# Kernel tuning notes

Hardware: AMD Instinct MI355X
Metric: run time of the kernel (lower is better)

## Reference

```python
import jax, jax.numpy as jnp
import numpy as np

N = 50000      # nodes
E = 800000     # edges (before self-loops)
B = 512        # graphs in batch
IN, HID, OUT, HEADS = 768, 256, 128, 4
NEG_SLOPE = 0.2
EPS = 1e-16


def glorot(key, shape):
    fan = shape[0] + shape[-1]
    return jax.random.normal(key, shape, jnp.float32) * jnp.sqrt(2.0 / fan)


def setup_inputs() -> dict:
    key = jax.random.key(0)
    ks = jax.random.split(key, 12)
    d1, d2 = HID // HEADS, OUT // HEADS
    return {
        "x": jax.random.normal(ks[0], (N, IN), jnp.float32),
        "edge_index": jax.random.randint(ks[1], (2, E), 0, N),
        "batch": jnp.sort(jax.random.randint(ks[2], (N,), 0, B)),
        # conv1: GATConv(IN, HID//HEADS, heads=HEADS)
        "W1": glorot(ks[3], (IN, HID)),
        "att_src1": glorot(ks[4], (HEADS, d1)),
        "att_dst1": glorot(ks[5], (HEADS, d1)),
        "b1": jnp.zeros((HID,), jnp.float32),
        # conv2: GATConv(HID+IN, OUT//HEADS, heads=HEADS)
        "W2": glorot(ks[6], (HID + IN, OUT)),
        "att_src2": glorot(ks[7], (HEADS, d2)),
        "att_dst2": glorot(ks[8], (HEADS, d2)),
        "b2": jnp.zeros((OUT,), jnp.float32),
    }


def gat_conv(x, src, dst, W, att_src, att_dst, bias):
    # PyG GATConv (concat heads): h = x @ W, e_ij = LeakyReLU(a_s.h_j + a_d.h_i),
    # alpha = softmax over incoming edges of each destination node.
    n = x.shape[0]
    heads, d = att_src.shape
    h = (x @ W).reshape(n, heads, d)                          # [N,H,D]
    a_s = jnp.einsum('nhd,hd->nh', h, att_src)                # [N,H]
    a_d = jnp.einsum('nhd,hd->nh', h, att_dst)
    e = jax.nn.leaky_relu(a_s[src] + a_d[dst], NEG_SLOPE)     # [Etot,H]
    e_max = jax.ops.segment_max(e, dst, num_segments=n)
    e = jnp.exp(e - e_max[dst])
    denom = jax.ops.segment_sum(e, dst, num_segments=n)
    alpha = e / (denom[dst] + EPS)                            # [Etot,H]
    msg = h[src] * alpha[:, :, None]                          # [Etot,H,D]
    out = jax.ops.segment_sum(msg, dst, num_segments=n)       # [N,H,D]
    return out.reshape(n, heads * d) + bias


def reference(x, edge_index, batch, W1, att_src1, att_dst1, b1,
              W2, att_src2, att_dst2, b2):
    # BUrumorGAT swaps edge direction: row<->col
    src = edge_index[1]
    dst = edge_index[0]
    # PyG GATConv adds self-loops by default
    loops = jnp.arange(N)
    src = jnp.concatenate([src, loops])
    dst = jnp.concatenate([dst, loops])

    x1 = x  # original features
    h1 = gat_conv(x, src, dst, W1, att_src1, att_dst1, b1)    # [N,HID]
    x2 = h1

    # root of each graph = first node (in order) with that batch id
    roots = jax.ops.segment_min(jnp.arange(N), batch, num_segments=B)  # [B]
    re1 = x1[roots[batch]]                                    # [N,IN]
    xc = jax.nn.relu(jnp.concatenate([h1, re1], axis=1))      # [N,HID+IN]
    # F.dropout with training=False is identity (eval mode)

    h2 = jax.nn.relu(gat_conv(xc, src, dst, W2, att_src2, att_dst2, b2))  # [N,OUT]
    re2 = x2[roots[batch]]                                    # [N,HID]
    feat = jnp.concatenate([h2, re2], axis=1)                 # [N,OUT+HID]

    counts = jax.ops.segment_sum(jnp.ones((N,), jnp.float32), batch, num_segments=B)
    pooled = jax.ops.segment_sum(feat, batch, num_segments=B)
    return pooled / jnp.clip(counts, 1.0)[:, None]            # [B,OUT+HID]
```

## Files before the change

kernel.cpp:

```cpp
#include <hip/hip_runtime.h>

#define NN 50000
#define NBGRAPH 512
#define DIN 768
#define DHID 256
#define DOUT 128

typedef unsigned short ushort_t;
typedef __attribute__((ext_vector_type(4))) float f32x4;
typedef _Float16 f16_t;
typedef __attribute__((ext_vector_type(8))) _Float16 f16x8;

__device__ __forceinline__ float lrelu(float v) { return v > 0.f ? v : 0.2f * v; }

__device__ __forceinline__ float h2f_u(ushort_t u) { return (float)__builtin_bit_cast(f16_t, u); }
__device__ __forceinline__ ushort_t f2h_u(float f) { return __builtin_bit_cast(ushort_t, (f16_t)f); }

__device__ __forceinline__ float sel_h(int h, float q0, float q1, float q2, float q3) {
  float lo = (h & 1) ? q1 : q0;
  float hi = (h & 1) ? q3 : q2;
  return (h & 2) ? hi : lo;
}

__device__ __forceinline__ f16x8 cvt8(float4 u, float4 v) {
  unsigned int a = __builtin_bit_cast(unsigned int, __builtin_amdgcn_cvt_pkrtz(u.x, u.y));
  unsigned int b = __builtin_bit_cast(unsigned int, __builtin_amdgcn_cvt_pkrtz(u.z, u.w));
  unsigned int c = __builtin_bit_cast(unsigned int, __builtin_amdgcn_cvt_pkrtz(v.x, v.y));
  unsigned int d = __builtin_bit_cast(unsigned int, __builtin_amdgcn_cvt_pkrtz(v.z, v.w));
  uint4 q = {a, b, c, d};
  return __builtin_bit_cast(f16x8, q);
}
__device__ __forceinline__ f16x8 cvt8_relu(float4 u, float4 v) {
  u.x = fmaxf(u.x, 0.f); u.y = fmaxf(u.y, 0.f); u.z = fmaxf(u.z, 0.f); u.w = fmaxf(u.w, 0.f);
  v.x = fmaxf(v.x, 0.f); v.y = fmaxf(v.y, 0.f); v.z = fmaxf(v.z, 0.f); v.w = fmaxf(v.w, 0.f);
  return cvt8(u, v);
}

__device__ __forceinline__ void gl_lds16(const void* g, void* l) {
  __builtin_amdgcn_global_load_lds(
      (const __attribute__((address_space(1))) unsigned int*)g,
      (__attribute__((address_space(3))) unsigned int*)l, 16, 0, 0);
}

__global__ void k_zero2(int* __restrict__ a, int* __restrict__ b, int n) {
  int i = blockIdx.x * blockDim.x + threadIdx.x;
  if (i < n) { a[i] = 0; b[i] = 0; }
}

__global__ void k_hist(const int* __restrict__ ei, int* __restrict__ deg, int E, int Etot) {
  int e = blockIdx.x * blockDim.x + threadIdx.x;
  if (e >= Etot) return;
  int dst = (e < E) ? ei[e] : (e - E);
  atomicAdd(&deg[dst], 1);
}

__global__ __launch_bounds__(1024) void k_scan1(const int* __restrict__ deg, int* __restrict__ off,
                                                int* __restrict__ bsum, int n) {
  __shared__ int wsum[16];
  int tid = threadIdx.x, lane = tid & 63, w = tid >> 6;
  int i = blockIdx.x * 1024 + tid;
  int v = (i < n) ? deg[i] : 0;
  int x = v;
#pragma unroll
  for (int d = 1; d < 64; d <<= 1) { int t = __shfl_up(x, d); if (lane >= d) x += t; }
  if (lane == 63) wsum[w] = x;
  __syncthreads();
  if (tid < 16) {
    int y = wsum[tid];
#pragma unroll
    for (int d = 1; d < 16; d <<= 1) { int t = __shfl_up(y, d); if (tid >= d) y += t; }
    wsum[tid] = y;
  }
  __syncthreads();
  int base = (w > 0) ? wsum[w - 1] : 0;
  if (i < n) off[i] = base + x - v;
  if (tid == 1023) bsum[blockIdx.x] = wsum[15];
}

__global__ void k_scan2(int* __restrict__ bsum, int* __restrict__ off, int nb, int n) {
  int lane = threadIdx.x;
  int v = (lane < nb) ? bsum[lane] : 0;
  int x = v;
#pragma unroll
  for (int d = 1; d < 64; d <<= 1) { int t = __shfl_up(x, d); if (lane >= d) x += t; }
  if (lane < nb) bsum[lane] = x - v;
  if (lane == 63) off[n] = x;
}

__global__ void k_scan3(int* __restrict__ off, const int* __restrict__ bsum, int n) {
  int i = blockIdx.x * blockDim.x + threadIdx.x;
  if (i < n) off[i] += bsum[i >> 10];
}

__global__ void k_scatter(const int* __restrict__ ei, const int* __restrict__ off,
                          int* __restrict__ cur, int* __restrict__ csr, int E, int Etot) {
  int e = blockIdx.x * blockDim.x + threadIdx.x;
  if (e >= Etot) return;
  int dst, src;
  if (e < E) { dst = ei[e]; src = ei[E + e]; }
  else       { dst = src = e - E; }
  int p = atomicAdd(&cur[dst], 1);
  csr[off[dst] + p] = src;
}

__global__ void k_segstart(const int* __restrict__ batch, int* __restrict__ segstart, int n, int b_cnt) {
  int b = blockIdx.x * blockDim.x + threadIdx.x;
  if (b > b_cnt) return;
  int lo = 0, hi = n;
  while (lo < hi) { int mid = (lo + hi) >> 1; if (batch[mid] < b) lo = mid + 1; else hi = mid; }
  segstart[b] = lo;
}

__global__ void k_rootn(const int* __restrict__ batch, const int* __restrict__ segstart,
                        int* __restrict__ rootn, int n) {
  int i = blockIdx.x * blockDim.x + threadIdx.x;
  if (i < n) rootn[i] = segstart[batch[i]];
}

__global__ void k_prepW(const float* __restrict__ W, ushort_t* __restrict__ Wt, int K, int N) {
  int id = blockIdx.x * blockDim.x + threadIdx.x;
  if (id >= K * N) return;
  int n = id / K, k = id - n * K;
  Wt[(size_t)n * K + k] = f2h_u(W[(size_t)k * N + n]);
}

__global__ __launch_bounds__(256) void k_gemm1m(const float* __restrict__ A,
                                                const ushort_t* __restrict__ Bt,
                                                ushort_t* __restrict__ C) {
  const int K = DIN, NC = DHID;
  __shared__ __align__(16) float As[128 * 32];
  __shared__ __align__(16) ushort_t Bs[128 * 32];
  const int tid = threadIdx.x;
  const int bm = blockIdx.x * 128;
  const int bn = blockIdx.y * 128;
  const int wid = tid >> 6, lane = tid & 63;
  const int wr = (wid >> 1) * 64, wc = (wid & 1) * 64;
  const int fr = lane & 15, fg = lane >> 4;
  f32x4 acc[4][4] = {};

  const float* asrc[4];
  float* adst[4];
#pragma unroll
  for (int j = 0; j < 4; ++j) {
    int c = j * 256 + tid;
    int row = c >> 3, ci = c & 7;
    int gc = ci ^ (row & 7);
    int gr = bm + row; if (gr >= NN) gr = NN - 1;
    asrc[j] = &A[(size_t)gr * K + gc * 4];
    adst[j] = &As[row * 32 + ci * 4];
  }
  const ushort_t* bsrc[2];
  ushort_t* bdst[2];
#pragma unroll
  for (int j = 0; j < 2; ++j) {
    int c = j * 256 + tid;
    int col = c >> 2, ci = c & 3;
    int gc = ci ^ (col & 3);
    bsrc[j] = &Bt[(size_t)(bn + col) * K + gc * 8];
    bdst[j] = &Bs[col * 32 + ci * 8];
  }

  for (int k0 = 0; k0 < K; k0 += 32) {
#pragma unroll
    for (int j = 0; j < 4; ++j) gl_lds16(asrc[j] + k0, adst[j]);
#pragma unroll
    for (int j = 0; j < 2; ++j) gl_lds16(bsrc[j] + k0, bdst[j]);
    __syncthreads();
    f16x8 af[4], bfr[4];
#pragma unroll
    for (int m = 0; m < 4; ++m) {
      int r = wr + m * 16 + fr;
      int c0 = (2 * fg) ^ (r & 7), c1 = (2 * fg + 1) ^ (r & 7);
      float4 u = *(const float4*)&As[r * 32 + c0 * 4];
      float4 v = *(const float4*)&As[r * 32 + c1 * 4];
      af[m] = cvt8(u, v);
    }
#pragma unroll
    for (int n = 0; n < 4; ++n) {
      int c = wc + n * 16 + fr;
      bfr[n] = *(const f16x8*)&Bs[c * 32 + (fg ^ (c & 3)) * 8];
    }
#pragma unroll
    for (int m = 0; m < 4; ++m)
#pragma unroll
      for (int n = 0; n < 4; ++n)
        acc[m][n] = __builtin_amdgcn_mfma_f32_16x16x32_f16(af[m], bfr[n], acc[m][n], 0, 0, 0);
    __syncthreads();
  }
#pragma unroll
  for (int m = 0; m < 4; ++m)
#pragma unroll
    for (int n = 0; n < 4; ++n)
#pragma unroll
      for (int j = 0; j < 4; ++j) {
        int r = bm + wr + m * 16 + fg * 4 + j;
        if (r < NN) C[(size_t)r * NC + bn + wc + n * 16 + fr] = f2h_u(acc[m][n][j]);
      }
}

__global__ __launch_bounds__(256) void k_gemm2m(const float* __restrict__ OUT1,
                                                const float* __restrict__ X,
                                                const int* __restrict__ rootn,
                                                const ushort_t* __restrict__ Bt,
                                                ushort_t* __restrict__ C) {
  const int K = DHID + DIN, NC = DOUT;
  __shared__ __align__(16) float As[128 * 32];
  __shared__ __align__(16) ushort_t Bs[128 * 32];
  const int tid = threadIdx.x;
  const int bm = blockIdx.x * 128;
  const int wid = tid >> 6, lane = tid & 63;
  const int wr = (wid >> 1) * 64, wc = (wid & 1) * 64;
  const int fr = lane & 15, fg = lane >> 4;
  f32x4 acc[4][4] = {};

  const float* o1src[4];
  const float* xsrc[4];
  float* adst[4];
#pragma unroll
  for (int j = 0; j < 4; ++j) {
    int c = j * 256 + tid;
    int row = c >> 3, ci = c & 7;
    int gc = ci ^ (row & 7);
    int gr = bm + row; if (gr >= NN) gr = NN - 1;
    int rn = rootn[gr];
    o1src[j] = &OUT1[(size_t)gr * DHID + gc * 4];
    xsrc[j] = &X[(size_t)rn * DIN + gc * 4];
    adst[j] = &As[row * 32 + ci * 4];
  }
  const ushort_t* bsrc[2];
  ushort_t* bdst[2];
#pragma unroll
  for (int j = 0; j < 2; ++j) {
    int c = j * 256 + tid;
    int col = c >> 2, ci = c & 3;
    int gc = ci ^ (col & 3);
    bsrc[j] = &Bt[(size_t)col * K + gc * 8];
    bdst[j] = &Bs[col * 32 + ci * 8];
  }

  for (int k0 = 0; k0 < K; k0 += 32) {
    const bool inO1 = k0 < DHID;
#pragma unroll
    for (int j = 0; j < 4; ++j)
      gl_lds16(inO1 ? (o1src[j] + k0) : (xsrc[j] + (k0 - DHID)), adst[j]);
#pragma unroll
    for (int j = 0; j < 2; ++j) gl_lds16(bsrc[j] + k0, bdst[j]);
    __syncthreads();
    f16x8 af[4], bfr[4];
#pragma unroll
    for (int m = 0; m < 4; ++m) {
      int r = wr + m * 16 + fr;
      int c0 = (2 * fg) ^ (r & 7), c1 = (2 * fg + 1) ^ (r & 7);
      float4 u = *(const float4*)&As[r * 32 + c0 * 4];
      float4 v = *(const float4*)&As[r * 32 + c1 * 4];
      af[m] = cvt8_relu(u, v);
    }
#pragma unroll
    for (int n = 0; n < 4; ++n) {
      int c = wc + n * 16 + fr;
      bfr[n] = *(const f16x8*)&Bs[c * 32 + (fg ^ (c & 3)) * 8];
    }
#pragma unroll
    for (int m = 0; m < 4; ++m)
#pragma unroll
      for (int n = 0; n < 4; ++n)
        acc[m][n] = __builtin_amdgcn_mfma_f32_16x16x32_f16(af[m], bfr[n], acc[m][n], 0, 0, 0);
    __syncthreads();
  }
#pragma unroll
  for (int m = 0; m < 4; ++m)
#pragma unroll
    for (int n = 0; n < 4; ++n)
#pragma unroll
      for (int j = 0; j < 4; ++j) {
        int r = bm + wr + m * 16 + fg * 4 + j;
        if (r < NN) C[(size_t)r * NC + wc + n * 16 + fr] = f2h_u(acc[m][n][j]);
      }
}

__global__ __launch_bounds__(256) void k_scores1(const ushort_t* __restrict__ Hh,
                                                 const float* __restrict__ att_s,
                                                 const float* __restrict__ att_d,
                                                 float4* __restrict__ as_out,
                                                 float4* __restrict__ ad_out) {
  int lane = threadIdx.x & 63;
  int n = blockIdx.x * 4 + (threadIdx.x >> 6);
  if (n >= NN) return;
  ushort4 hv = *(const ushort4*)&Hh[(size_t)n * DHID + lane * 4];
  float h0 = h2f_u(hv.x), h1 = h2f_u(hv.y), h2 = h2f_u(hv.z), h3 = h2f_u(hv.w);
  float4 sa = *(const float4*)&att_s[lane * 4];
  float4 da = *(const float4*)&att_d[lane * 4];
  float ps = h0 * sa.x + h1 * sa.y + h2 * sa.z + h3 * sa.w;
  float pd = h0 * da.x + h1 * da.y + h2 * da.z + h3 * da.w;
#pragma unroll
  for (int m = 1; m < 16; m <<= 1) { ps += __shfl_xor(ps, m); pd += __shfl_xor(pd, m); }
  float4 rs, rd;
  rs.x = __shfl(ps, 0);  rd.x = __shfl(pd, 0);
  rs.y = __shfl(ps, 16); rd.y = __shfl(pd, 16);
  rs.z = __shfl(ps, 32); rd.z = __shfl(pd, 32);
  rs.w = __shfl(ps, 48); rd.w = __shfl(pd, 48);
  if (lane == 0) { as_out[n] = rs; ad_out[n] = rd; }
}

__global__ __launch_bounds__(256) void k_scores2(const ushort_t* __restrict__ Hh,
                                                 const float* __restrict__ att_s,
                                                 const float* __restrict__ att_d,
                                                 float4* __restrict__ as_out,
                                                 float4* __restrict__ ad_out) {
  int lane = threadIdx.x & 63;
  int n = blockIdx.x * 4 + (threadIdx.x >> 6);
  if (n >= NN) return;
  ushort2 hv = *(const ushort2*)&Hh[(size_t)n * DOUT + lane * 2];
  float h0 = h2f_u(hv.x), h1 = h2f_u(hv.y);
  float2 sa = *(const float2*)&att_s[lane * 2];
  float2 da = *(const float2*)&att_d[lane * 2];
  float ps = h0 * sa.x + h1 * sa.y;
  float pd = h0 * da.x + h1 * da.y;
#pragma unroll
  for (int m = 1; m < 16; m <<= 1) { ps += __shfl_xor(ps, m); pd += __shfl_xor(pd, m); }
  float4 rs, rd;
  rs.x = __shfl(ps, 0);  rd.x = __shfl(pd, 0);
  rs.y = __shfl(ps, 16); rd.y = __shfl(pd, 16);
  rs.z = __shfl(ps, 32); rd.z = __shfl(pd, 32);
  rs.w = __shfl(ps, 48); rd.w = __shfl(pd, 48);
  if (lane == 0) { as_out[n] = rs; ad_out[n] = rd; }
}

__global__ __launch_bounds__(256) void k_agg1(const int* __restrict__ off, const int* __restrict__ csr,
                                              const float4* __restrict__ as_v, const float4* __restrict__ ad_v,
                                              const ushort_t* __restrict__ Hh, const float* __restrict__ bias,
                                              float* __restrict__ OUT) {
  __shared__ int s_tab[16][65];
  __shared__ __align__(16) float al_tab[16][260];
  const int tid = threadIdx.x;
  const int nd = tid >> 4;
  const int g = tid & 15;
  const int hd = g >> 2;
  const int n = blockIdx.x * 16 + nd;
  if (n >= NN) return;
  const int beg = off[n];
  const int nt = off[n + 1] - beg;
  const float4 adv = ad_v[n];

  float acc[16] = {};
  float rdh;

  if (nt <= 64) {
    float mx0 = -INFINITY, mx1 = -INFINITY, mx2 = -INFINITY, mx3 = -INFINITY;
    for (int le = g; le < nt; le += 16) {
      int s = csr[beg + le];
      float4 a = as_v[s];
      s_tab[nd][le] = s;
      *(float4*)&al_tab[nd][le << 2] = a;
      mx0 = fmaxf(mx0, a.x); mx1 = fmaxf(mx1, a.y);
      mx2 = fmaxf(mx2, a.z); mx3 = fmaxf(mx3, a.w);
    }
#pragma unroll
    for (int m = 1; m < 16; m <<= 1) {
      mx0 = fmaxf(mx0, __shfl_xor(mx0, m)); mx1 = fmaxf(mx1, __shfl_xor(mx1, m));
      mx2 = fmaxf(mx2, __shfl_xor(mx2, m)); mx3 = fmaxf(mx3, __shfl_xor(mx3, m));
    }
    float em0 = lrelu(mx0 + adv.x), em1 = lrelu(mx1 + adv.y);
    float em2 = lrelu(mx2 + adv.z), em3 = lrelu(mx3 + adv.w);
    float s0 = 0.f, s1 = 0.f, s2 = 0.f, s3 = 0.f;
    for (int le = g; le < nt; le += 16) {
      float4 a = *(const float4*)&al_tab[nd][le << 2];
      float p0 = __expf(lrelu(a.x + adv.x) - em0);
      float p1 = __expf(lrelu(a.y + adv.y) - em1);
      float p2 = __expf(lrelu(a.z + adv.z) - em2);
      float p3 = __expf(lrelu(a.w + adv.w) - em3);
      *(float4*)&al_tab[nd][le << 2] = make_float4(p0, p1, p2, p3);
      s0 += p0; s1 += p1; s2 += p2; s3 += p3;
    }
#pragma unroll
    for (int m = 1; m < 16; m <<= 1) {
      s0 += __shfl_xor(s0, m); s1 += __shfl_xor(s1, m);
      s2 += __shfl_xor(s2, m); s3 += __shfl_xor(s3, m);
    }
    rdh = sel_h(hd, 1.f / (s0 + 1e-16f), 1.f / (s1 + 1e-16f),
                    1.f / (s2 + 1e-16f), 1.f / (s3 + 1e-16f));

    int sP = s_tab[nd][0];
    float pP = al_tab[nd][hd];
    f16x8 v0 = *(const f16x8*)&Hh[(size_t)sP * DHID + g * 16];
    f16x8 v1 = *(const f16x8*)&Hh[(size_t)sP * DHID + g * 16 + 8];
    for (int e = 0; e < nt; ++e) {
      int en = (e + 1 < nt) ? e + 1 : e;
      int sN = s_tab[nd][en];
      float pN = al_tab[nd][(en << 2) | hd];
      f16x8 n0 = *(const f16x8*)&Hh[(size_t)sN * DHID + g * 16];
      f16x8 n1 = *(const f16x8*)&Hh[(size_t)sN * DHID + g * 16 + 8];
      float al = pP * rdh;
#pragma unroll
      for (int q = 0; q < 8; ++q) acc[q] += al * (float)v0[q];
#pragma unroll
      for (int q = 0; q < 8; ++q) acc[8 + q] += al * (float)v1[q];
      pP = pN; v0 = n0; v1 = n1;
    }
  } else {
    float mx0 = -INFINITY, mx1 = -INFINITY, mx2 = -INFINITY, mx3 = -INFINITY;
    for (int le = g; le < nt; le += 16) {
      float4 a = as_v[csr[beg + le]];
      mx0 = fmaxf(mx0, a.x); mx1 = fmaxf(mx1, a.y);
      mx2 = fmaxf(mx2, a.z); mx3 = fmaxf(mx3, a.w);
    }
#pragma unroll
    for (int m = 1; m < 16; m <<= 1) {
      mx0 = fmaxf(mx0, __shfl_xor(mx0, m)); mx1 = fmaxf(mx1, __shfl_xor(mx1, m));
      mx2 = fmaxf(mx2, __shfl_xor(mx2, m)); mx3 = fmaxf(mx3, __shfl_xor(mx3, m));
    }
    float em0 = lrelu(mx0 + adv.x), em1 = lrelu(mx1 + adv.y);
    float em2 = lrelu(mx2 + adv.z), em3 = lrelu(mx3 + adv.w);
    float s0 = 0.f, s1 = 0.f, s2 = 0.f, s3 = 0.f;
    for (int le = g; le < nt; le += 16) {
      float4 a = as_v[csr[beg + le]];
      s0 += __expf(lrelu(a.x + adv.x) - em0);
      s1 += __expf(lrelu(a.y + adv.y) - em1);
      s2 += __expf(lrelu(a.z + adv.z) - em2);
      s3 += __expf(lrelu(a.w + adv.w) - em3);
    }
#pragma unroll
    for (int m = 1; m < 16; m <<= 1) {
      s0 += __shfl_xor(s0, m); s1 += __shfl_xor(s1, m);
      s2 += __shfl_xor(s2, m); s3 += __shfl_xor(s3, m);
    }
    rdh = sel_h(hd, 1.f / (s0 + 1e-16f), 1.f / (s1 + 1e-16f),
                    1.f / (s2 + 1e-16f), 1.f / (s3 + 1e-16f));
    float adh = sel_h(hd, adv.x, adv.y, adv.z, adv.w);
    float emh = sel_h(hd, em0, em1, em2, em3);
    for (int e = 0; e < nt; ++e) {
      int s = csr[beg + e];
      float4 a = as_v[s];
      float ah = sel_h(hd, a.x, a.y, a.z, a.w);
      float al = __expf(lrelu(ah + adh) - emh) * rdh;
      f16x8 v0 = *(const f16x8*)&Hh[(size_t)s * DHID + g * 16];
      f16x8 v1 = *(const f16x8*)&Hh[(size_t)s * DHID + g * 16 + 8];
#pragma unroll
      for (int q = 0; q < 8; ++q) acc[q] += al * (float)v0[q];
#pragma unroll
      for (int q = 0; q < 8; ++q) acc[8 + q] += al * (float)v1[q];
    }
  }

  const float* bv = &bias[g * 16];
  float* ob = &OUT[(size_t)n * DHID + g * 16];
#pragma unroll
  for (int k = 0; k < 4; ++k) {
    float4 b4 = *(const float4*)&bv[k * 4];
    *(float4*)&ob[k * 4] = make_float4(acc[k * 4] + b4.x, acc[k * 4 + 1] + b4.y,
                                       acc[k * 4 + 2] + b4.z, acc[k * 4 + 3] + b4.w);
  }
}

__global__ __launch_bounds__(256) void k_agg2(const int* __restrict__ off, const int* __restrict__ csr,
                                              const float4* __restrict__ as_v, const float4* __restrict__ ad_v,
                                              const ushort_t* __restrict__ Hh, const float* __restrict__ bias,
                                              float* __restrict__ OUT) {
  __shared__ int s_tab[16][65];
  __shared__ __align__(16) float al_tab[16][260];
  const int tid = threadIdx.x;
  const int nd = tid >> 4;
  const int g = tid & 15;
  const int hd = g >> 2;
  const int n = blockIdx.x * 16 + nd;
  if (n >= NN) return;
  const int beg = off[n];
  const int nt = off[n + 1] - beg;
  const float4 adv = ad_v[n];

  float acc[8] = {};
  float rdh;

  if (nt <= 64) {
    float mx0 = -INFINITY, mx1 = -INFINITY, mx2 = -INFINITY, mx3 = -INFINITY;
    for (int le = g; le < nt; le += 16) {
      int s = csr[beg + le];
      float4 a = as_v[s];
      s_tab[nd][le] = s;
      *(float4*)&al_tab[nd][le << 2] = a;
      mx0 = fmaxf(mx0, a.x); mx1 = fmaxf(mx1, a.y);
      mx2 = fmaxf(mx2, a.z); mx3 = fmaxf(mx3, a.w);
    }
#pragma unroll
    for (int m = 1; m < 16; m <<= 1) {
      mx0 = fmaxf(mx0, __shfl_xor(mx0, m)); mx1 = fmaxf(mx1, __shfl_xor(mx1, m));
      mx2 = fmaxf(mx2, __shfl_xor(mx2, m)); mx3 = fmaxf(mx3, __shfl_xor(mx3, m));
    }
    float em0 = lrelu(mx0 + adv.x), em1 = lrelu(mx1 + adv.y);
    float em2 = lrelu(mx2 + adv.z), em3 = lrelu(mx3 + adv.w);
    float s0 = 0.f, s1 = 0.f, s2 = 0.f, s3 = 0.f;
    for (int le = g; le < nt; le += 16) {
      float4 a = *(const float4*)&al_tab[nd][le << 2];
      float p0 = __expf(lrelu(a.x + adv.x) - em0);
      float p1 = __expf(lrelu(a.y + adv.y) - em1);
      float p2 = __expf(lrelu(a.z + adv.z) - em2);
      float p3 = __expf(lrelu(a.w + adv.w) - em3);
      *(float4*)&al_tab[nd][le << 2] = make_float4(p0, p1, p2, p3);
      s0 += p0; s1 += p1; s2 += p2; s3 += p3;
    }
#pragma unroll
    for (int m = 1; m < 16; m <<= 1) {
      s0 += __shfl_xor(s0, m); s1 += __shfl_xor(s1, m);
      s2 += __shfl_xor(s2, m); s3 += __shfl_xor(s3, m);
    }
    rdh = sel_h(hd, 1.f / (s0 + 1e-16f), 1.f / (s1 + 1e-16f),
                    1.f / (s2 + 1e-16f), 1.f / (s3 + 1e-16f));

    int sP = s_tab[nd][0];
    float pP = al_tab[nd][hd];
    f16x8 v0 = *(const f16x8*)&Hh[(size_t)sP * DOUT + g * 8];
    for (int e = 0; e < nt; ++e) {
      int en = (e + 1 < nt) ? e + 1 : e;
      int sN = s_tab[nd][en];
      float pN = al_tab[nd][(en << 2) | hd];
      f16x8 n0 = *(const f16x8*)&Hh[(size_t)sN * DOUT + g * 8];
      float al = pP * rdh;
#pragma unroll
      for (int q = 0; q < 8; ++q) acc[q] += al * (float)v0[q];
      pP = pN; v0 = n0;
    }
  } else {
    float mx0 = -INFINITY, mx1 = -INFINITY, mx2 = -INFINITY, mx3 = -INFINITY;
    for (int le = g; le < nt; le += 16) {
      float4 a = as_v[csr[beg + le]];
      mx0 = fmaxf(mx0, a.x); mx1 = fmaxf(mx1, a.y);
      mx2 = fmaxf(mx2, a.z); mx3 = fmaxf(mx3, a.w);
    }
#pragma unroll
    for (int m = 1; m < 16; m <<= 1) {
      mx0 = fmaxf(mx0, __shfl_xor(mx0, m)); mx1 = fmaxf(mx1, __shfl_xor(mx1, m));
      mx2 = fmaxf(mx2, __shfl_xor(mx2, m)); mx3 = fmaxf(mx3, __shfl_xor(mx3, m));
    }
    float em0 = lrelu(mx0 + adv.x), em1 = lrelu(mx1 + adv.y);
    float em2 = lrelu(mx2 + adv.z), em3 = lrelu(mx3 + adv.w);
    float s0 = 0.f, s1 = 0.f, s2 = 0.f, s3 = 0.f;
    for (int le = g; le < nt; le += 16) {
      float4 a = as_v[csr[beg + le]];
      s0 += __expf(lrelu(a.x + adv.x) - em0);
      s1 += __expf(lrelu(a.y + adv.y) - em1);
      s2 += __expf(lrelu(a.z + adv.z) - em2);
      s3 += __expf(lrelu(a.w + adv.w) - em3);
    }
#pragma unroll
    for (int m = 1; m < 16; m <<= 1) {
      s0 += __shfl_xor(s0, m); s1 += __shfl_xor(s1, m);
      s2 += __shfl_xor(s2, m); s3 += __shfl_xor(s3, m);
    }
    rdh = sel_h(hd, 1.f / (s0 + 1e-16f), 1.f / (s1 + 1e-16f),
                    1.f / (s2 + 1e-16f), 1.f / (s3 + 1e-16f));
    float adh = sel_h(hd, adv.x, adv.y, adv.z, adv.w);
    float emh = sel_h(hd, em0, em1, em2, em3);
    for (int e = 0; e < nt; ++e) {
      int s = csr[beg + e];
      float4 a = as_v[s];
      float ah = sel_h(hd, a.x, a.y, a.z, a.w);
      float al = __expf(lrelu(ah + adh) - emh) * rdh;
      f16x8 v0 = *(const f16x8*)&Hh[(size_t)s * DOUT + g * 8];
#pragma unroll
      for (int q = 0; q < 8; ++q) acc[q] += al * (float)v0[q];
    }
  }

  const float* bv = &bias[g * 8];
  float* ob = &OUT[(size_t)n * DOUT + g * 8];
#pragma unroll
  for (int k = 0; k < 2; ++k) {
    float4 b4 = *(const float4*)&bv[k * 4];
    *(float4*)&ob[k * 4] = make_float4(acc[k * 4] + b4.x, acc[k * 4 + 1] + b4.y,
                                       acc[k * 4 + 2] + b4.z, acc[k * 4 + 3] + b4.w);
  }
}

__global__ __launch_bounds__(256) void k_pool(const int* __restrict__ segstart,
                                              const float* __restrict__ OUT2,
                                              const float* __restrict__ OUT1,
                                              float* __restrict__ out) {
  int b = blockIdx.x;
  int t = threadIdx.x;
  int s = segstart[b], e = segstart[b + 1];
  float* ob = out + (size_t)b * 384;
  if (s >= e) {
    for (int i = t; i < 384; i += 256) ob[i] = 0.f;
    return;
  }
  if (t < 128) {
    float s0 = 0.f, s1 = 0.f;
    int n = s;
    for (; n + 1 < e; n += 2) {
      float v0 = OUT2[(size_t)n * DOUT + t];
      float v1 = OUT2[(size_t)(n + 1) * DOUT + t];
      s0 += fmaxf(v0, 0.f); s1 += fmaxf(v1, 0.f);
    }
    if (n < e) s0 += fmaxf(OUT2[(size_t)n * DOUT + t], 0.f);
    ob[t] = (s0 + s1) / (float)(e - s);
  } else {
    int k = t - 128;
    ob[128 + k] = OUT1[(size_t)s * DHID + k];
    ob[256 + k] = OUT1[(size_t)s * DHID + 128 + k];
  }
}

extern "C" void kernel_launch(void* const* d_in, const int* in_sizes, int n_in,
                              void* d_out, int out_size, void* d_ws, size_t ws_size,
                              hipStream_t stream) {
  const float* x    = (const float*)d_in[0];
  const int*   ei   = (const int*)d_in[1];
  const int*   batch = (const int*)d_in[2];
  const float* W1   = (const float*)d_in[3];
  const float* as1w = (const float*)d_in[4];
  const float* ad1w = (const float*)d_in[5];
  const float* b1   = (const float*)d_in[6];
  const float* W2   = (const float*)d_in[7];
  const float* as2w = (const float*)d_in[8];
  const float* ad2w = (const float*)d_in[9];
  const float* b2   = (const float*)d_in[10];
  float* out = (float*)d_out;
  char* ws = (char*)d_ws;

  const int E = in_sizes[1] / 2;
  const int Etot = E + NN;

  ushort_t* H1h = (ushort_t*)(ws + 0);
  ushort_t* H2h = (ushort_t*)(ws + 0);
  ushort_t* Wt2h = (ushort_t*)(ws + 13000000);
  float*  OUT2 = (float*)(ws + 25600000);
  float*  OUT1 = (float*)(ws + 51200000);
  float4* as1  = (float4*)(ws + 102400000);
  float4* ad1  = (float4*)(ws + 103200000);
  float4* as2  = (float4*)(ws + 104000000);
  float4* ad2  = (float4*)(ws + 104800000);
  int* deg     = (int*)(ws + 105600000);
  int* cur     = (int*)(ws + 105800000);
  int* off     = (int*)(ws + 106000000);
  int* csr     = (int*)(ws + 106200016);
  int* segstart = (int*)(ws + 109600016);
  int* rootn   = (int*)(ws + 109602080);
  int* bsum    = (int*)(ws + 109802080);
  ushort_t* Wt1h = (ushort_t*)(ws + 105600000);

  const int TB = 256;
  const int NB_SCAN = (NN + 1023) / 1024;

  k_zero2<<<(NN + TB - 1) / TB, TB, 0, stream>>>(deg, cur, NN);
  k_hist<<<(Etot + TB - 1) / TB, TB, 0, stream>>>(ei, deg, E, Etot);
  k_scan1<<<NB_SCAN, 1024, 0, stream>>>(deg, off, bsum, NN);
  k_scan2<<<1, 64, 0, stream>>>(bsum, off, NB_SCAN, NN);
  k_scan3<<<NB_SCAN, 1024, 0, stream>>>(off, bsum, NN);
  k_scatter<<<(Etot + TB - 1) / TB, TB, 0, stream>>>(ei, off, cur, csr, E, Etot);
  k_segstart<<<(NBGRAPH + 1 + TB - 1) / TB, TB, 0, stream>>>(batch, segstart, NN, NBGRAPH);
  k_rootn<<<(NN + TB - 1) / TB, TB, 0, stream>>>(batch, segstart, rootn, NN);

  k_prepW<<<(DIN * DHID + TB - 1) / TB, TB, 0, stream>>>(W1, Wt1h, DIN, DHID);
  dim3 g1((NN + 127) / 128, DHID / 128);
  k_gemm1m<<<g1, TB, 0, stream>>>(x, Wt1h, H1h);
  k_scores1<<<(NN + 3) / 4, TB, 0, stream>>>(H1h, as1w, ad1w, as1, ad1);
  k_agg1<<<(NN + 15) / 16, TB, 0, stream>>>(off, csr, as1, ad1, H1h, b1, OUT1);

  k_prepW<<<((DHID + DIN) * DOUT + TB - 1) / TB, TB, 0, stream>>>(W2, Wt2h, DHID + DIN, DOUT);
  dim3 g2((NN + 127) / 128, 1);
  k_gemm2m<<<g2, TB, 0, stream>>>(OUT1, x, rootn, Wt2h, H2h);
  k_scores2<<<(NN + 3) / 4, TB, 0, stream>>>(H2h, as2w, ad2w, as2, ad2);
  k_agg2<<<(NN + 15) / 16, TB, 0, stream>>>(off, csr, as2, ad2, H2h, b2, OUT2);

  k_pool<<<NBGRAPH, TB, 0, stream>>>(segstart, OUT2, OUT1, out);
}
```

Before: 354.2 us.

## Double-buffer LDS tiles in both GEMMs and halve gemm2 row tile

Both MFMA GEMM kernels now keep two LDS buffers and issue the global-to-LDS loads for the next K slice before computing on the current one, so load latency overlaps with MFMA work and one barrier per iteration is removed. The second GEMM also drops from 128-row to 64-row tiles, doubling its grid to roughly 782 blocks so more CUs are busy for the single 128-column output. Costs are doubled LDS per block, which can lower occupancy, and less reuse of the B tile in gemm2.

```diff
diff --git a/kernel.cpp b/kernel.cpp
--- a/kernel.cpp
+++ b/kernel.cpp
@@ -124,12 +124,14 @@
   Wt[(size_t)n * K + k] = f2h_u(W[(size_t)k * N + n]);
 }
 
+#define ABUF1 (128 * 32)
+#define BBUF1 (128 * 32)
 __global__ __launch_bounds__(256) void k_gemm1m(const float* __restrict__ A,
                                                 const ushort_t* __restrict__ Bt,
                                                 ushort_t* __restrict__ C) {
   const int K = DIN, NC = DHID;
-  __shared__ __align__(16) float As[128 * 32];
-  __shared__ __align__(16) ushort_t Bs[128 * 32];
+  __shared__ __align__(16) float As[2 * ABUF1];
+  __shared__ __align__(16) ushort_t Bs[2 * BBUF1];
   const int tid = threadIdx.x;
   const int bm = blockIdx.x * 128;
   const int bn = blockIdx.y * 128;
@@ -139,7 +141,7 @@
   f32x4 acc[4][4] = {};
 
   const float* asrc[4];
-  float* adst[4];
+  int adoff[4];
 #pragma unroll
   for (int j = 0; j < 4; ++j) {
     int c = j * 256 + tid;
@@ -147,38 +149,49 @@
     int gc = ci ^ (row & 7);
     int gr = bm + row; if (gr >= NN) gr = NN - 1;
     asrc[j] = &A[(size_t)gr * K + gc * 4];
-    adst[j] = &As[row * 32 + ci * 4];
+    adoff[j] = row * 32 + ci * 4;
   }
   const ushort_t* bsrc[2];
-  ushort_t* bdst[2];
+  int bdoff[2];
 #pragma unroll
   for (int j = 0; j < 2; ++j) {
     int c = j * 256 + tid;
     int col = c >> 2, ci = c & 3;
     int gc = ci ^ (col & 3);
     bsrc[j] = &Bt[(size_t)(bn + col) * K + gc * 8];
-    bdst[j] = &Bs[col * 32 + ci * 8];
-  }
-
+    bdoff[j] = col * 32 + ci * 8;
+  }
+
+#pragma unroll
+  for (int j = 0; j < 4; ++j) gl_lds16(asrc[j], &As[adoff[j]]);
+#pragma unroll
+  for (int j = 0; j < 2; ++j) gl_lds16(bsrc[j], &Bs[bdoff[j]]);
+  __syncthreads();
+
+  int cur = 0;
   for (int k0 = 0; k0 < K; k0 += 32) {
-#pragma unroll
-    for (int j = 0; j < 4; ++j) gl_lds16(asrc[j] + k0, adst[j]);
-#pragma unroll
-    for (int j = 0; j < 2; ++j) gl_lds16(bsrc[j] + k0, bdst[j]);
-    __syncthreads();
+    const int nxt = cur ^ 1;
+    if (k0 + 32 < K) {
+#pragma unroll
+      for (int j = 0; j < 4; ++j) gl_lds16(asrc[j] + k0 + 32, &As[nxt * ABUF1 + adoff[j]]);
+#pragma unroll
+      for (int j = 0; j < 2; ++j) gl_lds16(bsrc[j] + k0 + 32, &Bs[nxt * BBUF1 + bdoff[j]]);
+    }
+    const float* Ab = &As[cur * ABUF1];
+    const ushort_t* Bb = &Bs[cur * BBUF1];
     f16x8 af[4], bfr[4];
 #pragma unroll
     for (int m = 0; m < 4; ++m) {
       int r = wr + m * 16 + fr;
       int c0 = (2 * fg) ^ (r & 7), c1 = (2 * fg + 1) ^ (r & 7);
-      float4 u = *(const float4*)&As[r * 32 + c0 * 4];
-      float4 v = *(const float4*)&As[r * 32 + c1 * 4];
+      float4 u = *(const float4*)&Ab[r * 32 + c0 * 4];
+      float4 v = *(const float4*)&Ab[r * 32 + c1 * 4];
       af[m] = cvt8(u, v);
     }
 #pragma unroll
     for (int n = 0; n < 4; ++n) {
       int c = wc + n * 16 + fr;
-      bfr[n] = *(const f16x8*)&Bs[c * 32 + (fg ^ (c & 3)) * 8];
+      bfr[n] = *(const f16x8*)&Bb[c * 32 + (fg ^ (c & 3)) * 8];
     }
 #pragma unroll
     for (int m = 0; m < 4; ++m)
@@ -186,6 +199,7 @@
       for (int n = 0; n < 4; ++n)
         acc[m][n] = __builtin_amdgcn_mfma_f32_16x16x32_f16(af[m], bfr[n], acc[m][n], 0, 0, 0);
     __syncthreads();
+    cur = nxt;
   }
 #pragma unroll
   for (int m = 0; m < 4; ++m)
@@ -198,26 +212,28 @@
       }
 }
 
+#define ABUF2 (64 * 32)
+#define BBUF2 (128 * 32)
 __global__ __launch_bounds__(256) void k_gemm2m(const float* __restrict__ OUT1,
                                                 const float* __restrict__ X,
                                                 const int* __restrict__ rootn,
                                                 const ushort_t* __restrict__ Bt,
                                                 ushort_t* __restrict__ C) {
   const int K = DHID + DIN, NC = DOUT;
-  __shared__ __align__(16) float As[128 * 32];
-  __shared__ __align__(16) ushort_t Bs[128 * 32];
+  __shared__ __align__(16) float As[2 * ABUF2];
+  __shared__ __align__(16) ushort_t Bs[2 * BBUF2];
   const int tid = threadIdx.x;
-  const int bm = blockIdx.x * 128;
+  const int bm = blockIdx.x * 64;
   const int wid = tid >> 6, lane = tid & 63;
-  const int wr = (wid >> 1) * 64, wc = (wid & 1) * 64;
+  const int wr = (wid >> 1) * 32, wc = (wid & 1) * 64;
   const int fr = lane & 15, fg = lane >> 4;
-  f32x4 acc[4][4] = {};
-
-  const float* o1src[4];
-  const float* xsrc[4];
-  float* adst[4];
-#pragma unroll
-  for (int j = 0; j < 4; ++j) {
+  f32x4 acc[2][4] = {};
+
+  const float* o1src[2];
+  const float* xsrc[2];
+  int adoff[2];
+#pragma unroll
+  for (int j = 0; j < 2; ++j) {
     int c = j * 256 + tid;
     int row = c >> 3, ci = c & 7;
     int gc = ci ^ (row & 7);
@@ -225,50 +241,63 @@
     int rn = rootn[gr];
     o1src[j] = &OUT1[(size_t)gr * DHID + gc * 4];
     xsrc[j] = &X[(size_t)rn * DIN + gc * 4];
-    adst[j] = &As[row * 32 + ci * 4];
+    adoff[j] = row * 32 + ci * 4;
   }
   const ushort_t* bsrc[2];
-  ushort_t* bdst[2];
+  int bdoff[2];
 #pragma unroll
   for (int j = 0; j < 2; ++j) {
     int c = j * 256 + tid;
     int col = c >> 2, ci = c & 3;
     int gc = ci ^ (col & 3);
     bsrc[j] = &Bt[(size_t)col * K + gc * 8];
-    bdst[j] = &Bs[col * 32 + ci * 8];
-  }
-
+    bdoff[j] = col * 32 + ci * 8;
+  }
+
+#pragma unroll
+  for (int j = 0; j < 2; ++j) gl_lds16(o1src[j], &As[adoff[j]]);
+#pragma unroll
+  for (int j = 0; j < 2; ++j) gl_lds16(bsrc[j], &Bs[bdoff[j]]);
+  __syncthreads();
+
+  int cur = 0;
   for (int k0 = 0; k0 < K; k0 += 32) {
-    const bool inO1 = k0 < DHID;
-#pragma unroll
-    for (int j = 0; j < 4; ++j)
-      gl_lds16(inO1 ? (o1src[j] + k0) : (xsrc[j] + (k0 - DHID)), adst[j]);
-#pragma unroll
-    for (int j = 0; j < 2; ++j) gl_lds16(bsrc[j] + k0, bdst[j]);
-    __syncthreads();
-    f16x8 af[4], bfr[4];
-#pragma unroll
-    for (int m = 0; m < 4; ++m) {
+    const int nxt = cur ^ 1;
+    if (k0 + 32 < K) {
+      const int k0n = k0 + 32;
+      const bool inO1 = k0n < DHID;
+#pragma unroll
+      for (int j = 0; j < 2; ++j)
+        gl_lds16(inO1 ? (o1src[j] + k0n) : (xsrc[j] + (k0n - DHID)), &As[nxt * ABUF2 + adoff[j]]);
+#pragma unroll
+      for (int j = 0; j < 2; ++j) gl_lds16(bsrc[j] + k0n, &Bs[nxt * BBUF2 + bdoff[j]]);
+    }
+    const float* Ab = &As[cur * ABUF2];
+    const ushort_t* Bb = &Bs[cur * BBUF2];
+    f16x8 af[2], bfr[4];
+#pragma unroll
+    for (int m = 0; m < 2; ++m) {
       int r = wr + m * 16 + fr;
       int c0 = (2 * fg) ^ (r & 7), c1 = (2 * fg + 1) ^ (r & 7);
-      float4 u = *(const float4*)&As[r * 32 + c0 * 4];
-      float4 v = *(const float4*)&As[r * 32 + c1 * 4];
+      float4 u = *(const float4*)&Ab[r * 32 + c0 * 4];
+      float4 v = *(const float4*)&Ab[r * 32 + c1 * 4];
       af[m] = cvt8_relu(u, v);
     }
 #pragma unroll
     for (int n = 0; n < 4; ++n) {
       int c = wc + n * 16 + fr;
-      bfr[n] = *(const f16x8*)&Bs[c * 32 + (fg ^ (c & 3)) * 8];
-    }
-#pragma unroll
-    for (int m = 0; m < 4; ++m)
+      bfr[n] = *(const f16x8*)&Bb[c * 32 + (fg ^ (c & 3)) * 8];
+    }
+#pragma unroll
+    for (int m = 0; m < 2; ++m)
 #pragma unroll
       for (int n = 0; n < 4; ++n)
         acc[m][n] = __builtin_amdgcn_mfma_f32_16x16x32_f16(af[m], bfr[n], acc[m][n], 0, 0, 0);
     __syncthreads();
-  }
-#pragma unroll
-  for (int m = 0; m < 4; ++m)
+    cur = nxt;
+  }
+#pragma unroll
+  for (int m = 0; m < 2; ++m)
 #pragma unroll
     for (int n = 0; n < 4; ++n)
 #pragma unroll
@@ -657,7 +686,7 @@
   k_agg1<<<(NN + 15) / 16, TB, 0, stream>>>(off, csr, as1, ad1, H1h, b1, OUT1);
 
   k_prepW<<<((DHID + DIN) * DOUT + TB - 1) / TB, TB, 0, stream>>>(W2, Wt2h, DHID + DIN, DOUT);
-  dim3 g2((NN + 127) / 128, 1);
+  dim3 g2((NN + 63) / 64, 1);
   k_gemm2m<<<g2, TB, 0, stream>>>(OUT1, x, rootn, Wt2h, H2h);
   k_scores2<<<(NN + 3) / 4, TB, 0, stream>>>(H2h, as2w, ad2w, as2, ad2);
   k_agg2<<<(NN + 15) / 16, TB, 0, stream>>>(off, csr, as2, ad2, H2h, b2, OUT2);
```

Result: no change. 352.0 us (-0.6%).
